# Performance work log

Measured on AMD Instinct MI355X. Metric: run time of the kernel, lower is better.

## Reference

```python
import jax, jax.numpy as jnp
import numpy as np

N = 50000      # nodes across the batched graph
E = 400000     # edges
F_IN = 128     # gnn_input_size
H = 3          # num_head
D = 64         # gnn_hidden_size
G = 64         # graphs in batch
P = 64         # pattern_input_size
NEG_GAT = 0.2  # GATv2Conv leaky_relu slope (dgl default)
NEG = 0.01     # nn.LeakyReLU default slope


def setup_inputs() -> dict:
    key = jax.random.key(0)
    ks = jax.random.split(key, 32)
    rn = lambda k, s, sc=0.05: jax.random.normal(k, s, dtype=jnp.float32) * sc
    HD = H * D
    return {
        "inputs": rn(ks[0], (N, F_IN), 1.0),
        "src": jax.random.randint(ks[1], (E,), 0, N),
        "dst": jax.random.randint(ks[2], (E,), 0, N),
        "graph_ids": jnp.sort(jax.random.randint(ks[3], (N,), 0, G)),
        "p1": rn(ks[4], (G, P), 1.0),
        "p2": rn(ks[5], (G, P), 1.0),
        "p3": rn(ks[6], (G, P), 1.0),
        # GATv2 layer params: fc_src, fc_dst, attn vector, bias
        "W1s": rn(ks[7], (F_IN, HD)), "W1d": rn(ks[8], (F_IN, HD)),
        "a1": rn(ks[9], (H, D)), "b1": rn(ks[10], (HD,)),
        "W2s": rn(ks[11], (HD, HD)), "W2d": rn(ks[12], (HD, HD)),
        "a2": rn(ks[13], (H, D)), "b2": rn(ks[14], (HD,)),
        "W3s": rn(ks[15], (HD, HD)), "W3d": rn(ks[16], (HD, HD)),
        "a3": rn(ks[17], (H, D)), "b3": rn(ks[18], (HD,)),
        # pattern branch (forward only uses ex_layer1 for all three inputs)
        "Wex": rn(ks[19], (P, 32)), "bex": rn(ks[20], (32,)),
        "Wpat": rn(ks[21], (96, P)), "bpat": rn(ks[22], (P,)),
        # classifier head
        "Wc1": rn(ks[23], (D + P, 64)), "bc1": rn(ks[24], (64,)),
        "Wc2": rn(ks[25], (64, 32)), "bc2": rn(ks[26], (32,)),
        "Wc3": rn(ks[27], (32, 2)), "bc3": rn(ks[28], (2,)),
    }


def _gatv2(x, src, dst, Ws, Wd, attn, bias):
    # dgl GATv2Conv (share_weights=False): e = a . leaky_relu(Ws x_u + Wd x_v)
    fs = (x @ Ws).reshape(N, H, D)
    fd = (x @ Wd).reshape(N, H, D)
    e = jax.nn.leaky_relu(fs[src] + fd[dst], NEG_GAT)            # [E,H,D]
    logits = jnp.einsum('ehd,hd->eh', e, attn)                   # [E,H]
    m = jax.ops.segment_max(logits, dst, num_segments=N)         # [N,H]
    m = jnp.where(jnp.isfinite(m), m, 0.0)                       # nodes w/o in-edges
    ex = jnp.exp(logits - m[dst])
    denom = jax.ops.segment_sum(ex, dst, num_segments=N)         # [N,H]
    alpha = ex / jnp.maximum(denom, 1e-9)[dst]                   # edge softmax
    out = jax.ops.segment_sum(alpha[:, :, None] * fs[src], dst, num_segments=N)
    return out + bias.reshape(1, H, D)                           # [N,H,D]


def reference(inputs, src, dst, graph_ids, p1, p2, p3,
              W1s, W1d, a1, b1, W2s, W2d, a2, b2, W3s, W3d, a3, b3,
              Wex, bex, Wpat, bpat, Wc1, bc1, Wc2, bc2, Wc3, bc3):
    h = _gatv2(inputs, src, dst, W1s, W1d, a1, b1).reshape(N, H * D)
    h = _gatv2(h, src, dst, W2s, W2d, a2, b2).reshape(N, H * D)
    h = _gatv2(h, src, dst, W3s, W3d, a3, b3).mean(axis=1)       # [N,D]
    # dgl.mean_nodes: per-graph mean over nodes
    sums = jax.ops.segment_sum(h, graph_ids, num_segments=G)
    cnts = jax.ops.segment_sum(jnp.ones((N,), h.dtype), graph_ids, num_segments=G)
    gnn_out = sums / jnp.maximum(cnts, 1.0)[:, None]             # [G,D]
    # pattern branch (ex_layer1 applied to all three, as in source)
    px = jnp.concatenate([p1 @ Wex + bex, p2 @ Wex + bex, p3 @ Wex + bex], axis=1)
    px = jax.nn.leaky_relu(px @ Wpat + bpat, NEG)                # [G,P]
    x = jnp.concatenate([gnn_out, px], axis=1)                   # [G,D+P]
    x = jax.nn.leaky_relu(x @ Wc1 + bc1, NEG)
    x = jax.nn.leaky_relu(x @ Wc2 + bc2, NEG)
    return x @ Wc3 + bc3                                         # [G,2]
```

## Files before the change

kernel.cpp:

```cpp
#include <hip/hip_runtime.h>
#include <cstdint>
#include <cstddef>

#define NN 50000
#define EE 400000
#define FIN 128
#define HH 3
#define DD 64
#define GG 64
#define PP 64
#define HD 192
#define EBL 1563

typedef short bf16x8 __attribute__((ext_vector_type(8)));
typedef float f32x4 __attribute__((ext_vector_type(4)));
typedef unsigned int u32x2 __attribute__((ext_vector_type(2)));

__device__ inline int wsumi(int v) {
#pragma unroll
    for (int m = 32; m > 0; m >>= 1) v += __shfl_xor(v, m, 64);
    return v;
}

__device__ inline float bf2f(unsigned short u) {
    union { unsigned int i; float f; } x; x.i = ((unsigned int)u) << 16; return x.f;
}
__device__ inline unsigned short f2bf(float f) {
    union { float f; unsigned int i; } x; x.f = f;
    unsigned int r = x.i + 0x7FFFu + ((x.i >> 16) & 1u);
    return (unsigned short)(r >> 16);
}

__device__ inline void unp2(unsigned int w, float& lo, float& hi) {
    union { unsigned int i; float f; } x;
    x.i = w << 16;          lo = x.f;
    x.i = w & 0xFFFF0000u;  hi = x.f;
}
__device__ inline void load4(const unsigned short* p, float* o) {
    u32x2 w = *(const u32x2*)p;
    unp2(w[0], o[0], o[1]);
    unp2(w[1], o[2], o[3]);
}

__device__ inline void loadrow(const unsigned short* __restrict__ FS, int u, int col,
                               float f[3][4]) {
    size_t bu = (size_t)u * HD + col;
#pragma unroll
    for (int h = 0; h < 3; h++) load4(&FS[bu + h * 64], f[h]);
}

__device__ inline void pack_one(const float* __restrict__ W, unsigned short* __restrict__ WP,
                                int id, int Kc) {
    int lane = id & 63;
    int kc = (id >> 6) % Kc;
    int ct = (id >> 6) / Kc;
    int n = ct * 16 + (lane & 15);
    int kb = kc * 32 + (lane >> 4) * 8;
#pragma unroll
    for (int j = 0; j < 8; j++)
        WP[(unsigned)id * 8 + j] = f2bf(W[(unsigned)(kb + j) * HD + n]);
}

#define IDS128 (12 * 4 * 64)
#define IDS192 (12 * 6 * 64)

__global__ void k_count_pack(const int* __restrict__ dst, int* __restrict__ counts,
                             const float* W1s, const float* W1d,
                             const float* W2s, const float* W2d,
                             const float* W3s, const float* W3d,
                             unsigned short* P1s, unsigned short* P1d,
                             unsigned short* P2s, unsigned short* P2d,
                             unsigned short* P3s, unsigned short* P3d) {
    int b = blockIdx.x;
    if (b < EBL) {
        int e = b * 256 + threadIdx.x;
        if (e < EE) atomicAdd(&counts[dst[e]], 1);
        return;
    }
    int idx = (b - EBL) * 256 + threadIdx.x;
    if (idx < IDS128) { pack_one(W1s, P1s, idx, 4); return; }
    idx -= IDS128;
    if (idx < IDS128) { pack_one(W1d, P1d, idx, 4); return; }
    idx -= IDS128;
    if (idx < IDS192) { pack_one(W2s, P2s, idx, 6); return; }
    idx -= IDS192;
    if (idx < IDS192) { pack_one(W2d, P2d, idx, 6); return; }
    idx -= IDS192;
    if (idx < IDS192) { pack_one(W3s, P3s, idx, 6); return; }
    idx -= IDS192;
    if (idx < IDS192) { pack_one(W3d, P3d, idx, 6); return; }
}

__global__ void k_scan_block(const int* __restrict__ in, int* __restrict__ out,
                             int* __restrict__ bsums) {
    int tid = threadIdx.x;
    int lane = tid & 63, w = tid >> 6;
    int i = blockIdx.x * 1024 + tid;
    int v = (i < NN) ? in[i] : 0;
    int s = v;
#pragma unroll
    for (int d = 1; d < 64; d <<= 1) {
        int t = __shfl_up(s, d, 64);
        if (lane >= d) s += t;
    }
    __shared__ int wsum[16], wpre[16];
    if (lane == 63) wsum[w] = s;
    __syncthreads();
    if (w == 0 && lane < 16) {
        int x = wsum[lane];
#pragma unroll
        for (int d = 1; d < 16; d <<= 1) {
            int t = __shfl_up(x, d, 64);
            if (lane >= d) x += t;
        }
        wpre[lane] = x - wsum[lane];
        if (lane == 15) bsums[blockIdx.x] = x;
    }
    __syncthreads();
    if (i < NN) out[i] = s - v + wpre[w];
}

__global__ void k_scan_add(int* __restrict__ row_ptr, const int* __restrict__ bsums, int nb) {
    __shared__ int sbase;
    int tid = threadIdx.x;
    if (tid < 64) {
        int v = (tid < blockIdx.x) ? bsums[tid] : 0;
        v = wsumi(v);
        if (tid == 0) sbase = v;
    }
    __syncthreads();
    int i = blockIdx.x * 1024 + tid;
    if (i < NN) row_ptr[i] += sbase;
    else if (i == NN) row_ptr[NN] = EE;
}

__global__ void k_scatter(const int* __restrict__ src, const int* __restrict__ dst,
                          const int* __restrict__ row_ptr, int* __restrict__ cursor,
                          int* __restrict__ csr_src) {
    int e = blockIdx.x * 256 + threadIdx.x;
    if (e >= EE) return;
    int v = dst[e];
    int pos = row_ptr[v] + atomicAdd(&cursor[v], 1);
    csr_src[pos] = src[e];
}

template <int K, bool BF16IN>
__global__ __launch_bounds__(256, 4) void k_gemm_mfma(const void* __restrict__ Xin,
                                                      const unsigned short* __restrict__ WPs,
                                                      const unsigned short* __restrict__ WPd,
                                                      unsigned short* __restrict__ FS,
                                                      unsigned short* __restrict__ FD) {
    constexpr int Kc = K / 32;
    constexpr int XW = K + 8;
    constexpr int BW = (XW > 200) ? XW : 200;
    __shared__ unsigned short smem[64 * BW];
    unsigned short (*xs)[XW]  = (unsigned short (*)[XW])smem;
    unsigned short (*cs)[200] = (unsigned short (*)[200])smem;
    int tid = threadIdx.x;
    int row0 = blockIdx.x * 64;
    int lane = tid & 63, wv = tid >> 6;
    int m = lane & 15, quad = lane >> 4;

    const unsigned short* WPx[2] = {WPs, WPd};
    unsigned short* OUTx[2] = {FS, FD};

    for (int half = 0; half < 2; half++) {
        if (BF16IN) {
            const unsigned short* XB = (const unsigned short*)Xin;
            for (int c = tid; c < 64 * K / 8; c += 256) {
                int r = c / (K / 8), kk = (c - r * (K / 8)) * 8;
                int row = row0 + r; if (row > NN - 1) row = NN - 1;
                *(bf16x8*)&xs[r][kk] = *(const bf16x8*)&XB[(unsigned)(row * K + kk)];
            }
        } else {
            const float* X = (const float*)Xin;
            for (int c = tid; c < 64 * K / 4; c += 256) {
                int r = c / (K / 4), k4 = (c - r * (K / 4)) * 4;
                int row = row0 + r; if (row > NN - 1) row = NN - 1;
                f32x4 v = *(const f32x4*)&X[(unsigned)(row * K + k4)];
                xs[r][k4 + 0] = f2bf(v[0]);
                xs[r][k4 + 1] = f2bf(v[1]);
                xs[r][k4 + 2] = f2bf(v[2]);
                xs[r][k4 + 3] = f2bf(v[3]);
            }
        }
        __syncthreads();

        f32x4 acc[4][3];
#pragma unroll
        for (int s = 0; s < 4; s++)
#pragma unroll
            for (int t = 0; t < 3; t++) acc[s][t] = (f32x4){0.f, 0.f, 0.f, 0.f};

        const unsigned short* wp = WPx[half];
        for (int kc = 0; kc < Kc; kc++) {
            bf16x8 b[3];
#pragma unroll
            for (int t = 0; t < 3; t++) {
                int c = wv * 3 + t;
                b[t] = *(const bf16x8*)&wp[(unsigned)(((c * Kc + kc) * 64 + lane) * 8)];
            }
#pragma unroll
            for (int s = 0; s < 4; s++) {
                bf16x8 a = *(const bf16x8*)&xs[s * 16 + m][kc * 32 + quad * 8];
#pragma unroll
                for (int t = 0; t < 3; t++)
                    acc[s][t] = __builtin_amdgcn_mfma_f32_16x16x32_bf16(a, b[t], acc[s][t], 0, 0, 0);
            }
        }
        __syncthreads();

#pragma unroll
        for (int s = 0; s < 4; s++)
#pragma unroll
            for (int t = 0; t < 3; t++) {
                int ct = wv * 3 + t;
#pragma unroll
                for (int r = 0; r < 4; r++)
                    cs[s * 16 + quad * 4 + r][ct * 16 + m] = f2bf(acc[s][t][r]);
            }
        __syncthreads();
        unsigned short* OUT = OUTx[half];
#pragma unroll
        for (int it = 0; it < 6; it++) {
            int c = tid + it * 256;
            int row = c / 24, ch = c - row * 24;
            int grow = row0 + row;
            if (grow < NN)
                *(bf16x8*)&OUT[(unsigned)(grow * HD + ch * 8)] =
                    *(const bf16x8*)&cs[row][ch * 8];
        }
        __syncthreads();
    }
}

template <bool FINAL>
__global__ __launch_bounds__(256) void k_node_gat(const int* __restrict__ row_ptr,
                                                  const int* __restrict__ csr_src,
                                                  const unsigned short* __restrict__ FS,
                                                  const unsigned short* __restrict__ FD,
                                                  const float* __restrict__ A,
                                                  const float* __restrict__ Bv,
                                                  unsigned short* __restrict__ XB,
                                                  float* __restrict__ H64) {
    int tid = threadIdx.x;
    int grp = tid >> 4, sub = tid & 15;
    int node = blockIdx.x * 16 + grp;
    int col = sub * 4;

    float a[3][4];
#pragma unroll
    for (int h = 0; h < 3; h++) {
        f32x4 av = *(const f32x4*)&A[h * 64 + col];
#pragma unroll
        for (int j = 0; j < 4; j++) a[h][j] = av[j];
    }

    int lo = row_ptr[node], hi = row_ptr[node + 1];

    float g[3][4];
#pragma unroll
    for (int h = 0; h < 3; h++) load4(&FD[(size_t)node * HD + h * 64 + col], g[h]);

    float r[3][4];
#pragma unroll
    for (int h = 0; h < 3; h++)
#pragma unroll
        for (int j = 0; j < 4; j++) r[h][j] = 0.f;
    float d0 = 0.f, d1 = 0.f, d2 = 0.f;

    auto accum = [&](const float f[3][4]) {
        float p0 = 0.f, p1 = 0.f, p2 = 0.f;
#pragma unroll
        for (int j = 0; j < 4; j++) {
            float s0 = f[0][j] + g[0][j]; s0 = fmaxf(s0, 0.2f * s0); p0 += s0 * a[0][j];
            float s1 = f[1][j] + g[1][j]; s1 = fmaxf(s1, 0.2f * s1); p1 += s1 * a[1][j];
            float s2 = f[2][j] + g[2][j]; s2 = fmaxf(s2, 0.2f * s2); p2 += s2 * a[2][j];
        }
#pragma unroll
        for (int m = 8; m > 0; m >>= 1) {
            p0 += __shfl_xor(p0, m, 64);
            p1 += __shfl_xor(p1, m, 64);
            p2 += __shfl_xor(p2, m, 64);
        }
        float w0 = __expf(p0), w1 = __expf(p1), w2 = __expf(p2);
#pragma unroll
        for (int j = 0; j < 4; j++) {
            r[0][j] += w0 * f[0][j];
            r[1][j] += w1 * f[1][j];
            r[2][j] += w2 * f[2][j];
        }
        d0 += w0; d1 += w1; d2 += w2;
    };

    if (hi > lo) {
        int last = hi - 1;
        float fA[3][4], fB[3][4], fC[3][4];
        loadrow(FS, csr_src[lo], col, fA);
        loadrow(FS, csr_src[lo + 1 <= last ? lo + 1 : last], col, fB);
        for (int e = lo; e < hi; e += 3) {
            int eC = e + 2 <= last ? e + 2 : last;
            int eA = e + 3 <= last ? e + 3 : last;
            int eB = e + 4 <= last ? e + 4 : last;
            int uC = csr_src[eC], uA = csr_src[eA], uB = csr_src[eB];
            loadrow(FS, uC, col, fC);
            accum(fA);
            loadrow(FS, uA, col, fA);
            if (e + 1 < hi) accum(fB);
            loadrow(FS, uB, col, fB);
            if (e + 2 < hi) accum(fC);
        }
    }

    float b[3][4];
#pragma unroll
    for (int h = 0; h < 3; h++) {
        f32x4 bv = *(const f32x4*)&Bv[h * 64 + col];
#pragma unroll
        for (int j = 0; j < 4; j++) b[h][j] = bv[j];
    }

    float q0 = fmaxf(d0, 1e-9f), q1 = fmaxf(d1, 1e-9f), q2 = fmaxf(d2, 1e-9f);
    if (FINAL) {
        f32x4 m;
#pragma unroll
        for (int j = 0; j < 4; j++)
            m[j] = (r[0][j] / q0 + b[0][j] + r[1][j] / q1 + b[1][j] +
                    r[2][j] / q2 + b[2][j]) * (1.f / 3.f);
        *(f32x4*)&H64[(size_t)node * 64 + col] = m;
    } else {
        float qq[3] = {q0, q1, q2};
#pragma unroll
        for (int h = 0; h < 3; h++) {
            unsigned short o0 = f2bf(r[h][0] / qq[h] + b[h][0]);
            unsigned short o1 = f2bf(r[h][1] / qq[h] + b[h][1]);
            unsigned short o2 = f2bf(r[h][2] / qq[h] + b[h][2]);
            unsigned short o3 = f2bf(r[h][3] / qq[h] + b[h][3]);
            u32x2 w;
            w[0] = (unsigned)o0 | ((unsigned)o1 << 16);
            w[1] = (unsigned)o2 | ((unsigned)o3 << 16);
            *(u32x2*)&XB[(size_t)node * HD + h * 64 + col] = w;
        }
    }
}

__global__ __launch_bounds__(256) void k_graph_mean(const float* __restrict__ H64,
                                                    const int* __restrict__ gids,
                                                    float* __restrict__ gsum,
                                                    int* __restrict__ gcnt) {
    int g = blockIdx.x >> 2, q = blockIdx.x & 3;
    int lo, hi;
    {
        int a = 0, b = NN;
        while (a < b) { int m = (a + b) >> 1; if (gids[m] < g) a = m + 1; else b = m; }
        lo = a;
        b = NN;
        while (a < b) { int m = (a + b) >> 1; if (gids[m] < g + 1) a = m + 1; else b = m; }
        hi = a;
    }
    int len = hi - lo;
    int qlen = (len + 3) >> 2;
    int s = lo + q * qlen;
    int e = s + qlen; if (e > hi) e = hi;
    int lane = threadIdx.x & 63, wv = threadIdx.x >> 6;

    float acc = 0.f;
    for (int v = s + wv; v < e; v += 4)
        acc += H64[(size_t)v * 64 + lane];
    __shared__ float red[4][64];
    red[wv][lane] = acc;
    __syncthreads();
    if (wv == 0) {
        float t = red[0][lane] + red[1][lane] + red[2][lane] + red[3][lane];
        if (e > s) {
            atomicAdd(&gsum[g * 64 + lane], t);
            if (lane == 0) atomicAdd(&gcnt[g], e - s);
        }
    }
}

__global__ __launch_bounds__(128) void k_head(const float* __restrict__ gsum, const int* __restrict__ gcnt,
                                              const float* __restrict__ p1, const float* __restrict__ p2,
                                              const float* __restrict__ p3,
                                              const float* __restrict__ Wex, const float* __restrict__ bex,
                                              const float* __restrict__ Wpat, const float* __restrict__ bpat,
                                              const float* __restrict__ Wc1, const float* __restrict__ bc1,
                                              const float* __restrict__ Wc2, const float* __restrict__ bc2,
                                              const float* __restrict__ Wc3, const float* __restrict__ bc3,
                                              float* __restrict__ out) {
    int g = blockIdx.x;
    int tid = threadIdx.x;
    __shared__ float pbuf[192];
    __shared__ float ex[96], xc[128], t1[64], t2[32];

    if (tid < 64)       pbuf[tid] = p1[g * 64 + tid];
    else if (tid < 128) pbuf[tid] = p2[g * 64 + tid - 64];
    if (tid < 64)       pbuf[128 + tid] = p3[g * 64 + tid];
    if (tid >= 64 && tid < 128)
        xc[tid - 64] = gsum[g * 64 + tid - 64] / fmaxf((float)gcnt[g], 1.f);
    __syncthreads();
    if (tid < 96) {
        int jj = tid & 31;
        const float* pp = &pbuf[(tid >> 5) * 64];
        float acc = bex[jj];
        for (int k = 0; k < 64; k++) acc += pp[k] * Wex[k * 32 + jj];
        ex[tid] = acc;
    }
    __syncthreads();
    if (tid < 64) {
        float acc = bpat[tid];
        for (int k = 0; k < 96; k++) acc += ex[k] * Wpat[k * 64 + tid];
        xc[64 + tid] = acc > 0.f ? acc : 0.01f * acc;
    }
    __syncthreads();
    if (tid < 64) {
        float acc = bc1[tid];
        for (int k = 0; k < 128; k++) acc += xc[k] * Wc1[k * 64 + tid];
        t1[tid] = acc > 0.f ? acc : 0.01f * acc;
    }
    __syncthreads();
    if (tid < 32) {
        float acc = bc2[tid];
        for (int k = 0; k < 64; k++) acc += t1[k] * Wc2[k * 32 + tid];
        t2[tid] = acc > 0.f ? acc : 0.01f * acc;
    }
    __syncthreads();
    if (tid < 2) {
        float acc = bc3[tid];
        for (int k = 0; k < 32; k++) acc += t2[k] * Wc3[k * 2 + tid];
        out[g * 2 + tid] = acc;
    }
}

extern "C" void kernel_launch(void* const* d_in, const int* in_sizes, int n_in,
                              void* d_out, int out_size, void* d_ws, size_t ws_size,
                              hipStream_t stream) {
    const float* X0  = (const float*)d_in[0];
    const int*   src = (const int*)d_in[1];
    const int*   dst = (const int*)d_in[2];
    const int*   gid = (const int*)d_in[3];
    const float* p1  = (const float*)d_in[4];
    const float* p2  = (const float*)d_in[5];
    const float* p3  = (const float*)d_in[6];
    const float* W1s = (const float*)d_in[7],  *W1d = (const float*)d_in[8];
    const float* a1  = (const float*)d_in[9],  *b1  = (const float*)d_in[10];
    const float* W2s = (const float*)d_in[11], *W2d = (const float*)d_in[12];
    const float* a2  = (const float*)d_in[13], *b2  = (const float*)d_in[14];
    const float* W3s = (const float*)d_in[15], *W3d = (const float*)d_in[16];
    const float* a3  = (const float*)d_in[17], *b3  = (const float*)d_in[18];
    const float* Wex = (const float*)d_in[19], *bex = (const float*)d_in[20];
    const float* Wpat= (const float*)d_in[21], *bpat= (const float*)d_in[22];
    const float* Wc1 = (const float*)d_in[23], *bc1 = (const float*)d_in[24];
    const float* Wc2 = (const float*)d_in[25], *bc2 = (const float*)d_in[26];
    const float* Wc3 = (const float*)d_in[27], *bc3 = (const float*)d_in[28];
    float* out = (float*)d_out;

    char* ws = (char*)d_ws;
    size_t off = 0;
    auto alloc = [&](size_t bytes) -> char* {
        char* p = ws + off;
        off = (off + bytes + 255) & ~(size_t)255;
        return p;
    };
    unsigned short* FS = (unsigned short*)alloc((size_t)NN * HD * 2);
    unsigned short* FD = (unsigned short*)alloc((size_t)NN * HD * 2);
    unsigned short* XB = (unsigned short*)alloc((size_t)NN * HD * 2);
    float*          H64= (float*)alloc((size_t)NN * 64 * 4);
    unsigned short* P1s = (unsigned short*)alloc((size_t)192 * 192 * 2);
    unsigned short* P1d = (unsigned short*)alloc((size_t)192 * 192 * 2);
    unsigned short* P2s = (unsigned short*)alloc((size_t)192 * 192 * 2);
    unsigned short* P2d = (unsigned short*)alloc((size_t)192 * 192 * 2);
    unsigned short* P3s = (unsigned short*)alloc((size_t)192 * 192 * 2);
    unsigned short* P3d = (unsigned short*)alloc((size_t)192 * 192 * 2);
    int* row_ptr = (int*)alloc((size_t)(NN + 1) * 4);
    int* csr_src = (int*)alloc((size_t)EE * 4);
    int* bsums   = (int*)alloc(64 * 4);
    char* zbase = ws + off;
    int*   counts = (int*)alloc((size_t)NN * 4);
    int*   cursor = (int*)alloc((size_t)NN * 4);
    float* gsum   = (float*)alloc((size_t)GG * 64 * 4);
    int*   gcnt   = (int*)alloc((size_t)GG * 4);
    size_t zbytes = (size_t)((ws + off) - zbase);

    hipMemsetAsync(zbase, 0, zbytes, stream);

    int nb  = (NN + 1023) / 1024;
    {
        int packbl = (2 * IDS128 + 4 * IDS192 + 255) / 256;
        k_count_pack<<<EBL + packbl, 256, 0, stream>>>(dst, counts,
                                                       W1s, W1d, W2s, W2d, W3s, W3d,
                                                       P1s, P1d, P2s, P2d, P3s, P3d);
    }
    k_scan_block<<<nb, 1024, 0, stream>>>(counts, row_ptr, bsums);
    k_scan_add<<<nb, 1024, 0, stream>>>(row_ptr, bsums, nb);
    k_scatter<<<EBL, 256, 0, stream>>>(src, dst, row_ptr, cursor, csr_src);

    int gblk = (NN + 63) / 64;
    int nblk = NN / 16;

    k_gemm_mfma<128, false><<<gblk, 256, 0, stream>>>(X0, P1s, P1d, FS, FD);
    k_node_gat<false><<<nblk, 256, 0, stream>>>(row_ptr, csr_src, FS, FD, a1, b1, XB, nullptr);
    k_gemm_mfma<192, true><<<gblk, 256, 0, stream>>>(XB, P2s, P2d, FS, FD);
    k_node_gat<false><<<nblk, 256, 0, stream>>>(row_ptr, csr_src, FS, FD, a2, b2, XB, nullptr);
    k_gemm_mfma<192, true><<<gblk, 256, 0, stream>>>(XB, P3s, P3d, FS, FD);
    k_node_gat<true><<<nblk, 256, 0, stream>>>(row_ptr, csr_src, FS, FD, a3, b3, nullptr, H64);

    k_graph_mean<<<GG * 4, 256, 0, stream>>>(H64, gid, gsum, gcnt);
    k_head<<<GG, 128, 0, stream>>>(gsum, gcnt, p1, p2, p3, Wex, bex, Wpat, bpat,
                                   Wc1, bc1, Wc2, bc2, Wc3, bc3, out);
}
```

Measured before the change: 368.0 us.

## Sort nodes by in-degree bucket to balance node GAT aggregation work

Adds a degree histogram and counting-sort pass that builds a permutation of nodes grouped by in-degree (capped at 63), and the node GAT kernels process nodes in that order. The aim is for 16-lane groups within a wave and block to handle nodes of similar degree, which reduces divergence and tail imbalance in the per-node edge loop. The cost is two small extra kernels plus an indirect node lookup. It also loses the spatial locality of contiguous node rows for FD loads and output stores.

```diff
diff --git a/kernel.cpp b/kernel.cpp
--- a/kernel.cpp
+++ b/kernel.cpp
@@ -89,6 +89,37 @@
     if (idx < IDS192) { pack_one(W3s, P3s, idx, 6); return; }
     idx -= IDS192;
     if (idx < IDS192) { pack_one(W3d, P3d, idx, 6); return; }
+}
+
+__global__ void k_dhist(const int* __restrict__ counts, int* __restrict__ dhist) {
+    int i = blockIdx.x * 256 + threadIdx.x;
+    if (i < NN) {
+        int b = counts[i]; if (b > 63) b = 63;
+        atomicAdd(&dhist[b], 1);
+    }
+}
+
+__global__ void k_dperm(const int* __restrict__ counts, const int* __restrict__ dhist,
+                        int* __restrict__ dcur, int* __restrict__ perm) {
+    __shared__ int sbase[64];
+    int tid = threadIdx.x;
+    if (tid < 64) {
+        int x = dhist[tid];
+        int s = x;
+#pragma unroll
+        for (int d = 1; d < 64; d <<= 1) {
+            int t = __shfl_up(s, d, 64);
+            if (tid >= d) s += t;
+        }
+        sbase[tid] = s - x;
+    }
+    __syncthreads();
+    int i = blockIdx.x * 256 + tid;
+    if (i < NN) {
+        int b = counts[i]; if (b > 63) b = 63;
+        int pos = sbase[b] + atomicAdd(&dcur[b], 1);
+        perm[pos] = i;
+    }
 }
 
 __global__ void k_scan_block(const int* __restrict__ in, int* __restrict__ out,
@@ -235,7 +266,8 @@
 }
 
 template <bool FINAL>
-__global__ __launch_bounds__(256) void k_node_gat(const int* __restrict__ row_ptr,
+__global__ __launch_bounds__(256) void k_node_gat(const int* __restrict__ perm,
+                                                  const int* __restrict__ row_ptr,
                                                   const int* __restrict__ csr_src,
                                                   const unsigned short* __restrict__ FS,
                                                   const unsigned short* __restrict__ FD,
@@ -245,7 +277,7 @@
                                                   float* __restrict__ H64) {
     int tid = threadIdx.x;
     int grp = tid >> 4, sub = tid & 15;
-    int node = blockIdx.x * 16 + grp;
+    int node = perm[blockIdx.x * 16 + grp];
     int col = sub * 4;
 
     float a[3][4];
@@ -475,9 +507,12 @@
     int* row_ptr = (int*)alloc((size_t)(NN + 1) * 4);
     int* csr_src = (int*)alloc((size_t)EE * 4);
     int* bsums   = (int*)alloc(64 * 4);
+    int* perm    = (int*)alloc((size_t)NN * 4);
     char* zbase = ws + off;
     int*   counts = (int*)alloc((size_t)NN * 4);
     int*   cursor = (int*)alloc((size_t)NN * 4);
+    int*   dhist  = (int*)alloc(64 * 4);
+    int*   dcur   = (int*)alloc(64 * 4);
     float* gsum   = (float*)alloc((size_t)GG * 64 * 4);
     int*   gcnt   = (int*)alloc((size_t)GG * 4);
     size_t zbytes = (size_t)((ws + off) - zbase);
@@ -485,6 +520,7 @@
     hipMemsetAsync(zbase, 0, zbytes, stream);
 
     int nb  = (NN + 1023) / 1024;
+    int nbl = (NN + 255) / 256;
     {
         int packbl = (2 * IDS128 + 4 * IDS192 + 255) / 256;
         k_count_pack<<<EBL + packbl, 256, 0, stream>>>(dst, counts,
@@ -493,17 +529,19 @@
     }
     k_scan_block<<<nb, 1024, 0, stream>>>(counts, row_ptr, bsums);
     k_scan_add<<<nb, 1024, 0, stream>>>(row_ptr, bsums, nb);
+    k_dhist<<<nbl, 256, 0, stream>>>(counts, dhist);
     k_scatter<<<EBL, 256, 0, stream>>>(src, dst, row_ptr, cursor, csr_src);
+    k_dperm<<<nbl, 256, 0, stream>>>(counts, dhist, dcur, perm);
 
     int gblk = (NN + 63) / 64;
     int nblk = NN / 16;
 
     k_gemm_mfma<128, false><<<gblk, 256, 0, stream>>>(X0, P1s, P1d, FS, FD);
-    k_node_gat<false><<<nblk, 256, 0, stream>>>(row_ptr, csr_src, FS, FD, a1, b1, XB, nullptr);
+    k_node_gat<false><<<nblk, 256, 0, stream>>>(perm, row_ptr, csr_src, FS, FD, a1, b1, XB, nullptr);
     k_gemm_mfma<192, true><<<gblk, 256, 0, stream>>>(XB, P2s, P2d, FS, FD);
-    k_node_gat<false><<<nblk, 256, 0, stream>>>(row_ptr, csr_src, FS, FD, a2, b2, XB, nullptr);
+    k_node_gat<false><<<nblk, 256, 0, stream>>>(perm, row_ptr, csr_src, FS, FD, a2, b2, XB, nullptr);
     k_gemm_mfma<192, true><<<gblk, 256, 0, stream>>>(XB, P3s, P3d, FS, FD);
-    k_node_gat<true><<<nblk, 256, 0, stream>>>(row_ptr, csr_src, FS, FD, a3, b3, nullptr, H64);
+    k_node_gat<true><<<nblk, 256, 0, stream>>>(perm, row_ptr, csr_src, FS, FD, a3, b3, nullptr, H64);
 
     k_graph_mean<<<GG * 4, 256, 0, stream>>>(H64, gid, gsum, gcnt);
     k_head<<<GG, 128, 0, stream>>>(gsum, gcnt, p1, p2, p3, Wex, bex, Wpat, bpat,
```

New measurement: 709.5 us. 1.93x slower.
